# Optimization experiments

Measured on AMD Instinct MI355X. Metric: run time of the kernel, lower is better.

## Reference

```python
import jax, jax.numpy as jnp
import numpy as np

B, D, N, H = 16, 512, 4096, 4
HD = D // H  # head_dim = 128


def conv1(x, w, b):
    # 1x1 Conv1d == per-position matmul. x: (b, Cin, L), w: (Cout, Cin), b: (Cout,)
    return jnp.einsum('oi,bin->bon', w, x) + b[:, None]


def ln_c(x, g, b, eps=1e-5):
    # TransLN: LayerNorm over the channel axis (axis=1) at every position.
    m = jnp.mean(x, axis=1, keepdims=True)
    v = jnp.var(x, axis=1, keepdims=True)
    return (x - m) * jax.lax.rsqrt(v + eps) * g[:, None] + b[:, None]


def gelu(x):
    return jax.nn.gelu(x, approximate=False)  # torch nn.GELU default = exact erf


def setup_inputs() -> dict:
    key = jax.random.key(0)
    ks = iter(jax.random.split(key, 40))

    def rn(*shape):
        return jax.random.normal(next(ks), shape, jnp.float32) * 0.02

    inp = {
        'group_token': jax.random.normal(next(ks), (B, D, 2), jnp.float32),
        'x': jax.random.normal(next(ks), (B, D, N), jnp.float32),
        # mlp_s: Mlp(2, D//2) -> Conv1d(2, D//2), GELU, Conv1d(D//2, 2)
        'ws1_w': rn(D // 2, 2), 'ws1_b': jnp.zeros(D // 2, jnp.float32),
        'ws2_w': rn(2, D // 2), 'ws2_b': jnp.zeros(2, jnp.float32),
        # mlp_c: Mlp(D, 4D)
        'wc1_w': rn(4 * D, D), 'wc1_b': jnp.zeros(4 * D, jnp.float32),
        'wc2_w': rn(D, 4 * D), 'wc2_b': jnp.zeros(D, jnp.float32),
        # proj q/k/v: Conv1d(D, D)
        'q_w': rn(D, D), 'q_b': jnp.zeros(D, jnp.float32),
        'k_w': rn(D, D), 'k_b': jnp.zeros(D, jnp.float32),
        'v_w': rn(D, D), 'v_b': jnp.zeros(D, jnp.float32),
        'merge_w': rn(D, D), 'merge_b': jnp.zeros(D, jnp.float32),
        # mlp = MLP([2D, 2D, D], do_bn=False): Conv1d(2D,2D), GELU, Conv1d(2D,D)
        'm1_w': rn(2 * D, 2 * D), 'm1_b': jnp.zeros(2 * D, jnp.float32),
        'm2_w': rn(D, 2 * D), 'm2_b': jnp.zeros(D, jnp.float32),
        # norm0 / norm1 LayerNorm(D)
        'n0_g': jnp.ones(D, jnp.float32), 'n0_b': jnp.zeros(D, jnp.float32),
        'n1_g': jnp.ones(D, jnp.float32), 'n1_b': jnp.zeros(D, jnp.float32),
        # grouping: D->64->16->4->2 with TransLN+GELU between, softmax(axis=1)
        'g1_w': rn(64, D), 'g1_b': jnp.zeros(64, jnp.float32),
        'gl1_g': jnp.ones(64, jnp.float32), 'gl1_b': jnp.zeros(64, jnp.float32),
        'g2_w': rn(16, 64), 'g2_b': jnp.zeros(16, jnp.float32),
        'gl2_g': jnp.ones(16, jnp.float32), 'gl2_b': jnp.zeros(16, jnp.float32),
        'g3_w': rn(4, 16), 'g3_b': jnp.zeros(4, jnp.float32),
        'gl3_g': jnp.ones(4, jnp.float32), 'gl3_b': jnp.zeros(4, jnp.float32),
        'g4_w': rn(2, 4), 'g4_b': jnp.zeros(2, jnp.float32),
    }
    return inp


def reference(group_token, x, ws1_w, ws1_b, ws2_w, ws2_b, wc1_w, wc1_b, wc2_w, wc2_b,
              q_w, q_b, k_w, k_b, v_w, v_b, merge_w, merge_b,
              m1_w, m1_b, m2_w, m2_b, n0_g, n0_b, n1_g, n1_b,
              g1_w, g1_b, gl1_g, gl1_b, g2_w, g2_b, gl2_g, gl2_b,
              g3_w, g3_b, gl3_g, gl3_b, g4_w, g4_b):
    b = x.shape[0]
    # group_token: (b, D, 2)
    gt_t = jnp.swapaxes(group_token, 1, 2)                    # (b, 2, D)
    s = conv1(gelu(conv1(gt_t, ws1_w, ws1_b)), ws2_w, ws2_b)  # (b, 2, D)
    gt = group_token + jnp.swapaxes(s, 1, 2)
    gt = gt + conv1(gelu(conv1(gt, wc1_w, wc1_b)), wc2_w, wc2_b)

    # projections; torch view(b, head_dim, heads, -1) splits channels as (HD, H)
    q = conv1(x, q_w, q_b).reshape(b, HD, H, N)
    k = conv1(gt, k_w, k_b).reshape(b, HD, H, 2)
    v = conv1(gt, v_w, v_b).reshape(b, HD, H, 2)

    attn = jax.nn.softmax(jnp.einsum('bdhn,bdhm->bhnm', q, k) * (HD ** -0.5), axis=-1)
    out = jnp.einsum('bhnm,bdhm->bdhn', attn, v).reshape(b, D, N)
    out = conv1(out, merge_w, merge_b)

    h = jnp.concatenate([x, ln_c(out, n0_g, n0_b)], axis=1)   # (b, 2D, N)
    h = conv1(gelu(conv1(h, m1_w, m1_b)), m2_w, m2_b)         # (b, D, N)
    xd = x + ln_c(h, n1_g, n1_b)

    g = gelu(ln_c(conv1(xd, g1_w, g1_b), gl1_g, gl1_b))
    g = gelu(ln_c(conv1(g, g2_w, g2_b), gl2_g, gl2_b))
    g = gelu(ln_c(conv1(g, g3_w, g3_b), gl3_g, gl3_b))
    g = jax.nn.softmax(conv1(g, g4_w, g4_b), axis=1)          # (b, 2, N)
    return g[:, 0, :]                                         # (b, N)
```

## Files before the change

### kernel.cpp

```cpp
#include <hip/hip_runtime.h>
#include <math.h>

typedef unsigned short u16;
typedef unsigned int u32;
typedef __attribute__((ext_vector_type(8))) short bfrag;
typedef __attribute__((ext_vector_type(4))) float f32x4;

__device__ __forceinline__ float gelu_f(float x){
  return 0.5f * x * (1.0f + erff(x * 0.70710678118654752440f));
}
__device__ __forceinline__ u16 f2bf(float f){
  union { float f; unsigned int i; } c; c.f = f;
  unsigned int i = c.i;
  return (u16)((i + 0x7FFFu + ((i >> 16) & 1u)) >> 16);
}
__device__ __forceinline__ float bf2f(u16 u){
  union { unsigned int i; float f; } c; c.i = ((unsigned int)u) << 16; return c.f;
}

__device__ __forceinline__ void gload_lds16(const u16* g, u16* l){
  __builtin_amdgcn_global_load_lds(
      (const __attribute__((address_space(1))) u32*)(g),
      (__attribute__((address_space(3))) u32*)(l),
      16, 0, 0);
}

struct F8 { float v[8]; };
__device__ __forceinline__ F8 load8f(const float* p){
  float4 a = *(const float4*)p; float4 b = *(const float4*)(p + 4);
  F8 r; r.v[0]=a.x; r.v[1]=a.y; r.v[2]=a.z; r.v[3]=a.w;
  r.v[4]=b.x; r.v[5]=b.y; r.v[6]=b.z; r.v[7]=b.w; return r;
}

#define PRE_STRIDE 4624

__global__ __launch_bounds__(256) void k0a_mlps(
    const float* __restrict__ gtok,
    const float* __restrict__ ws1_w, const float* __restrict__ ws1_b,
    const float* __restrict__ ws2_w, const float* __restrict__ ws2_b,
    float* __restrict__ GT1)
{
  __shared__ float sw1[256][2]; __shared__ float sb1[256];
  __shared__ float sw2[2][256];
  const int b = blockIdx.x;
  const int t = threadIdx.x;
  sw1[t][0] = ws1_w[2*t]; sw1[t][1] = ws1_w[2*t+1];
  sb1[t] = ws1_b[t];
  sw2[0][t] = ws2_w[t]; sw2[1][t] = ws2_w[256+t];
  __syncthreads();
  const int j = blockIdx.y*256 + t;
  const float a0 = gtok[b*1024 + 2*j], a1 = gtok[b*1024 + 2*j + 1];
  float s0 = ws2_b[0], s1 = ws2_b[1];
  #pragma unroll 4
  for (int o = 0; o < 256; ++o){
    float h = gelu_f(sw1[o][0]*a0 + sw1[o][1]*a1 + sb1[o]);
    s0 += sw2[0][o]*h; s1 += sw2[1][o]*h;
  }
  GT1[b*1024 + 2*j]     = a0 + s0;
  GT1[b*1024 + 2*j + 1] = a1 + s1;
}

__global__ __launch_bounds__(256) void k0b_fc1(
    const float* __restrict__ GT1,
    const float* __restrict__ wc1_w, const float* __restrict__ wc1_b,
    float* __restrict__ HID)
{
  __shared__ float g[1024];
  const int b = blockIdx.x;
  const int t = threadIdx.x;
  for (int i = t; i < 1024; i += 256) g[i] = GT1[b*1024 + i];
  __syncthreads();
  const int o = blockIdx.y*256 + t;
  const float* wr = wc1_w + (size_t)o*512;
  float acc0 = wc1_b[o], acc1 = acc0;
  for (int d = 0; d < 512; d += 8){
    F8 w = load8f(wr + d);
    #pragma unroll
    for (int i = 0; i < 8; ++i){
      acc0 += w.v[i]*g[(d+i)*2];
      acc1 += w.v[i]*g[(d+i)*2+1];
    }
  }
  HID[b*4096 + o]        = gelu_f(acc0);
  HID[b*4096 + 2048 + o] = gelu_f(acc1);
}

__global__ __launch_bounds__(256) void k0c_fc2(
    const float* __restrict__ GT1, const float* __restrict__ HID,
    const float* __restrict__ wc2_w, const float* __restrict__ wc2_b,
    float* __restrict__ GT2)
{
  __shared__ float h0[2048], h1[2048];
  const int b = blockIdx.x;
  const int t = threadIdx.x;
  for (int i = t; i < 2048; i += 256){
    h0[i] = HID[b*4096 + i]; h1[i] = HID[b*4096 + 2048 + i];
  }
  __syncthreads();
  const int d = blockIdx.y*256 + t;
  const float* wr = wc2_w + (size_t)d*2048;
  float acc0 = wc2_b[d], acc1 = acc0;
  for (int o = 0; o < 2048; o += 8){
    F8 w = load8f(wr + o);
    #pragma unroll
    for (int i = 0; i < 8; ++i){
      acc0 += w.v[i]*h0[o+i];
      acc1 += w.v[i]*h1[o+i];
    }
  }
  GT2[b*1024 + 2*d]     = GT1[b*1024 + 2*d]     + acc0;
  GT2[b*1024 + 2*d + 1] = GT1[b*1024 + 2*d + 1] + acc1;
}

__global__ __launch_bounds__(256) void k0d_kv(
    const float* __restrict__ GT2,
    const float* __restrict__ k_w,
    const float* __restrict__ v_w, const float* __restrict__ v_b,
    float* __restrict__ DK, float* __restrict__ DV, float* __restrict__ V1L)
{
  __shared__ float g[1024];
  const int b = blockIdx.x;
  const int t = threadIdx.x;
  for (int i = t; i < 1024; i += 256) g[i] = GT2[b*1024 + i];
  __syncthreads();
  const int c = blockIdx.y*256 + t;
  const float* kr = k_w + (size_t)c*512;
  const float* vr = v_w + (size_t)c*512;
  float k0a=0.f,k1a=0.f,v0a=0.f,v1a=0.f;
  for (int d = 0; d < 512; d += 8){
    F8 kw = load8f(kr + d); F8 vw = load8f(vr + d);
    #pragma unroll
    for (int i = 0; i < 8; ++i){
      float g0 = g[(d+i)*2], g1 = g[(d+i)*2+1];
      k0a += kw.v[i]*g0; k1a += kw.v[i]*g1;
      v0a += vw.v[i]*g0; v1a += vw.v[i]*g1;
    }
  }
  DK[b*512 + c]  = k0a - k1a;
  DV[b*512 + c]  = v0a - v1a;
  V1L[b*512 + c] = v1a + v_b[c];
}

__global__ __launch_bounds__(256) void k0e_qpre(
    const float* __restrict__ DK,
    const float* __restrict__ q_w, const float* __restrict__ q_b,
    float* __restrict__ PRE)
{
  __shared__ float dkl[512];
  const int b = blockIdx.x;
  const int t = threadIdx.x;
  for (int i = t; i < 512; i += 256) dkl[i] = DK[b*512 + i];
  __syncthreads();
  const int i = blockIdx.y*256 + t;
  float w0=0.f,w1=0.f,w2=0.f,w3=0.f;
  for (int c = 0; c < 512; c += 4){
    w0 += dkl[c]  *q_w[(size_t)(c)  *512 + i];
    w1 += dkl[c+1]*q_w[(size_t)(c+1)*512 + i];
    w2 += dkl[c+2]*q_w[(size_t)(c+2)*512 + i];
    w3 += dkl[c+3]*q_w[(size_t)(c+3)*512 + i];
  }
  float* P = PRE + (size_t)b * PRE_STRIDE;
  P[0*512+i]=w0; P[1*512+i]=w1; P[2*512+i]=w2; P[3*512+i]=w3;
  if (blockIdx.y == 0 && t < 4){
    float bsum = 0.f;
    for (int c = t; c < 512; c += 4) bsum += dkl[c]*q_b[c];
    P[2048 + t] = bsum;
  }
}

__global__ __launch_bounds__(256) void k0f_mpre(
    const float* __restrict__ DV, const float* __restrict__ V1L,
    const float* __restrict__ merge_w, const float* __restrict__ merge_b,
    float* __restrict__ PRE)
{
  __shared__ float dvl[512], v1ll[512];
  const int b = blockIdx.x;
  const int t = threadIdx.x;
  for (int i = t; i < 512; i += 256){
    dvl[i] = DV[b*512 + i]; v1ll[i] = V1L[b*512 + i];
  }
  __syncthreads();
  const int r = blockIdx.y*256 + t;
  const float* mw = merge_w + (size_t)r*512;
  float ab = merge_b[r];
  float mh[4] = {0.f,0.f,0.f,0.f};
  for (int c = 0; c < 512; c += 8){
    F8 w = load8f(mw + c);
    #pragma unroll
    for (int i = 0; i < 8; ++i){
      ab += w.v[i]*v1ll[c+i];
      mh[i&3] += w.v[i]*dvl[c+i];
    }
  }
  float* P = PRE + (size_t)b * PRE_STRIDE;
  P[2064 + r] = ab;
  *(float4*)&P[2576 + r*4] = make_float4(mh[0],mh[1],mh[2],mh[3]);
}

__global__ __launch_bounds__(256) void kcvt(const float* __restrict__ s,
                                            u16* __restrict__ d, int n8)
{
  int g = blockIdx.x*256 + threadIdx.x;
  if (g >= n8) return;
  F8 v = load8f(s + (size_t)g*8);
  u16 o[8];
  #pragma unroll
  for (int i=0;i<8;++i) o[i] = f2bf(v.v[i]);
  *(uint4*)(d + (size_t)g*8) = *(uint4*)o;
}

__global__ __launch_bounds__(256) void kcvt_dup(const float* __restrict__ g1w,
                                                u16* __restrict__ out)
{
  int idx = blockIdx.x*256 + threadIdx.x;
  int r = idx >> 10, k = idx & 1023;
  out[idx] = f2bf(g1w[r*512 + (k & 511)]);
}

__global__ __launch_bounds__(256) void k1_fused(
    const float* __restrict__ x, const float* __restrict__ PRE,
    const float* __restrict__ n0_g, const float* __restrict__ n0_b,
    int j0_global, u16* __restrict__ XYbT)
{
  __shared__ float wd[4][512];
  __shared__ float bs[512];
  __shared__ float Mm[512][4];
  __shared__ float gam[512], bet[512];
  __shared__ float beta4[4];
  __shared__ float part[4][2][128];
  __shared__ float pstat[2][2][128];
  const int tid = threadIdx.x;
  const int cid = tid & 127;
  const int half = tid >> 7;
  const int jl = blockIdx.x*128 + cid;
  const int jg = j0_global + jl;
  const int b = jg >> 12, n = jg & 4095;
  const float* P = PRE + (size_t)b * PRE_STRIDE;
  for (int i = tid; i < 2048; i += 256) wd[i>>9][i&511] = P[i];
  if (tid < 4) beta4[tid] = P[2048 + tid];
  for (int i = tid; i < 512; i += 256){
    bs[i] = P[2064 + i]; gam[i] = n0_g[i]; bet[i] = n0_b[i];
  }
  for (int i = tid; i < 2048; i += 256) Mm[i>>2][i&3] = P[2576 + i];
  __syncthreads();
  const float* xc = x + (size_t)b*2097152 + n;
  u16* col = XYbT + (size_t)jl*1024;
  const int ibase = half*256;
  float l0=0.f, l1=0.f, l2=0.f, l3=0.f;
  for (int i0 = 0; i0 < 256; i0 += 8){
    u16 ob[8];
    #pragma unroll
    for (int m = 0; m < 8; ++m){
      int i = ibase + i0 + m;
      float xv = xc[(size_t)i*4096];
      ob[m] = f2bf(xv);
      l0 += wd[0][i]*xv; l1 += wd[1][i]*xv;
      l2 += wd[2][i]*xv; l3 += wd[3][i]*xv;
    }
    *(uint4*)&col[ibase + i0] = *(uint4*)ob;
  }
  part[0][half][cid] = l0; part[1][half][cid] = l1;
  part[2][half][cid] = l2; part[3][half][cid] = l3;
  __syncthreads();
  l0 = part[0][0][cid] + part[0][1][cid] + beta4[0];
  l1 = part[1][0][cid] + part[1][1][cid] + beta4[1];
  l2 = part[2][0][cid] + part[2][1][cid] + beta4[2];
  l3 = part[3][0][cid] + part[3][1][cid] + beta4[3];
  const float sc = 0.0883883476483184405f;
  float p0 = 1.f/(1.f+expf(-sc*l0));
  float p1 = 1.f/(1.f+expf(-sc*l1));
  float p2 = 1.f/(1.f+expf(-sc*l2));
  float p3 = 1.f/(1.f+expf(-sc*l3));
  float s=0.f, s2=0.f;
  for (int c = ibase; c < ibase + 256; ++c){
    float m = bs[c] + Mm[c][0]*p0 + Mm[c][1]*p1 + Mm[c][2]*p2 + Mm[c][3]*p3;
    s += m; s2 += m*m;
  }
  pstat[0][half][cid] = s; pstat[1][half][cid] = s2;
  __syncthreads();
  s  = pstat[0][0][cid] + pstat[0][1][cid];
  s2 = pstat[1][0][cid] + pstat[1][1][cid];
  float mean = s*(1.f/512.f);
  float rs = rsqrtf(s2*(1.f/512.f) - mean*mean + 1e-5f);
  for (int c0 = ibase; c0 < ibase + 256; c0 += 8){
    u16 ob[8];
    #pragma unroll
    for (int m = 0; m < 8; ++m){
      int c = c0 + m;
      float v = bs[c] + Mm[c][0]*p0 + Mm[c][1]*p1 + Mm[c][2]*p2 + Mm[c][3]*p3;
      ob[m] = f2bf((v - mean)*rs*gam[c] + bet[c]);
    }
    *(uint4*)&col[512 + c0] = *(uint4*)ob;
  }
}

__global__ __launch_bounds__(256) void mfma_gemm_p(
    const u16* __restrict__ Wb, const float* __restrict__ bias,
    const u16* __restrict__ XT, int K, int M,
    u16* __restrict__ Out, int do_gelu, int log2nbi)
{
  __shared__ __align__(16) u16 SH[2][8192];
  const int tid = threadIdx.x;
  const int lane = tid & 63;
  const int wv = __builtin_amdgcn_readfirstlane(tid >> 6);
  const int id = blockIdx.x;
  const int bi = (id >> 3) & ((1 << log2nbi) - 1);
  const int bj = (id & 7) + 8 * (id >> (3 + log2nbi));
  const int roff = (wv >> 1) * 64;
  const int noff = (wv & 1) * 64;
  const int lm = lane & 15, quad = lane >> 4;

  f32x4 acc[4][4];
  #pragma unroll
  for (int i=0;i<4;++i){
    #pragma unroll
    for (int j=0;j<4;++j) acc[i][j] = (f32x4){0.f,0.f,0.f,0.f};
  }

  const int r16 = lane >> 2;
  const int kc  = (lane & 3) * 8;
  const u16* aG = Wb + (size_t)(bi*128 + wv*32 + r16)*K + kc;
  const u16* bG = XT + (size_t)(bj*128 + wv*32 + r16)*1024 + kc;
  const int aOff = wv*1024;
  const int bOff = 4096 + wv*1024;

#define GP_STAGE(base, kk) do { \
    gload_lds16(aG + (kk),                 (base) + aOff); \
    gload_lds16(aG + (size_t)16*K + (kk),  (base) + aOff + 512); \
    gload_lds16(bG + (kk),                 (base) + bOff); \
    gload_lds16(bG + 16*1024 + (kk),       (base) + bOff + 512); \
  } while(0)

#define GP_COMPUTE(base) do { \
    bfrag av[4], bv[4]; \
    _Pragma("unroll") \
    for (int i=0;i<4;++i) \
      av[i] = *(const bfrag*)&(base)[(roff + 16*i + lm)*32 + quad*8]; \
    _Pragma("unroll") \
    for (int j=0;j<4;++j) \
      bv[j] = *(const bfrag*)&(base)[4096 + (noff + 16*j + lm)*32 + quad*8]; \
    _Pragma("unroll") \
    for (int i=0;i<4;++i){ \
      _Pragma("unroll") \
      for (int j=0;j<4;++j) \
        acc[i][j] = __builtin_amdgcn_mfma_f32_16x16x32_bf16(av[i], bv[j], acc[i][j], 0,0,0); \
    } \
  } while(0)

  u16* cur = &SH[0][0];
  u16* nxt = &SH[1][0];
  GP_STAGE(cur, 0);
  for (int k0 = 0; k0 + 32 < K; k0 += 32){
    GP_STAGE(nxt, k0 + 32);
    asm volatile("s_waitcnt vmcnt(4)" ::: "memory");
    __builtin_amdgcn_s_barrier();
    __builtin_amdgcn_sched_barrier(0);
    GP_COMPUTE(cur);
    __builtin_amdgcn_sched_barrier(0);
    __builtin_amdgcn_s_barrier();
    u16* t = cur; cur = nxt; nxt = t;
  }
  asm volatile("s_waitcnt vmcnt(0)" ::: "memory");
  __builtin_amdgcn_s_barrier();
  __builtin_amdgcn_sched_barrier(0);
  GP_COMPUTE(cur);
  __syncthreads();
#undef GP_STAGE
#undef GP_COMPUTE

  u16* Tt = &SH[0][0];
  #pragma unroll
  for (int p = 0; p < 2; ++p){
    if ((wv & 1) == p){
      #pragma unroll
      for (int i=0;i<4;++i){
        float4 bb = *(const float4*)&bias[bi*128 + roff + 16*i + quad*4];
        float b4[4] = {bb.x,bb.y,bb.z,bb.w};
        #pragma unroll
        for (int j=0;j<4;++j){
          int colr = 16*j + lm;
          #pragma unroll
          for (int s2=0;s2<2;++s2){
            float v0 = acc[i][j][2*s2]   + b4[2*s2];
            float v1 = acc[i][j][2*s2+1] + b4[2*s2+1];
            if (do_gelu){ v0 = gelu_f(v0); v1 = gelu_f(v1); }
            unsigned int dw = (unsigned int)f2bf(v0) | ((unsigned int)f2bf(v1) << 16);
            *(unsigned int*)&Tt[colr*136 + roff + 16*i + quad*4 + 2*s2] = dw;
          }
        }
      }
    }
    __syncthreads();
    {
      int c = tid >> 2, q = tid & 3;
      u16* dst = Out + (size_t)(bj*128 + p*64 + c)*M + bi*128 + q*32;
      const u16* src = &Tt[c*136 + q*32];
      #pragma unroll
      for (int m=0;m<2;++m){
        *(uint4*)(dst + m*8)      = *(const uint4*)(src + m*8);
        *(uint4*)(dst + 16 + m*8) = *(const uint4*)(src + 16 + m*8);
      }
    }
    __syncthreads();
  }
}

__global__ __launch_bounds__(256) void mfma_g64(
    const u16* __restrict__ Wg, const float* __restrict__ bias,
    const u16* __restrict__ XT, u16* __restrict__ Out)
{
  __shared__ __align__(16) u16 SH[2][10240];
  const int tid = threadIdx.x;
  const int lane = tid & 63;
  const int wv = __builtin_amdgcn_readfirstlane(tid >> 6);
  const int bj = blockIdx.x;
  const int lm = lane & 15, quad = lane >> 4;

  f32x4 acc[4][4];
  #pragma unroll
  for (int i=0;i<4;++i){
    #pragma unroll
    for (int j=0;j<4;++j) acc[i][j] = (f32x4){0.f,0.f,0.f,0.f};
  }
  const int r16 = lane >> 2;
  const int kc  = (lane & 3) * 8;
  const u16* aG = Wg + (size_t)(wv*16 + r16)*1024 + kc;
  const u16* bG = XT + (size_t)(bj*256 + wv*64 + r16)*1024 + kc;
  const int aOff = wv*512;
  const int bOff = 2048 + wv*2048;

#define G64_STAGE(base, kk) do { \
    gload_lds16(aG + (kk), (base) + aOff); \
    _Pragma("unroll") \
    for (int g = 0; g < 4; ++g) \
      gload_lds16(bG + (size_t)(g*16)*1024 + (kk), (base) + bOff + g*512); \
  } while(0)

#define G64_COMPUTE(base) do { \
    bfrag av[4], bv[4]; \
    _Pragma("unroll") \
    for (int i=0;i<4;++i) \
      av[i] = *(const bfrag*)&(base)[(16*i + lm)*32 + quad*8]; \
    _Pragma("unroll") \
    for (int j=0;j<4;++j) \
      bv[j] = *(const bfrag*)&(base)[2048 + (wv*64 + 16*j + lm)*32 + quad*8]; \
    _Pragma("unroll") \
    for (int i=0;i<4;++i){ \
      _Pragma("unroll") \
      for (int j=0;j<4;++j) \
        acc[i][j] = __builtin_amdgcn_mfma_f32_16x16x32_bf16(av[i], bv[j], acc[i][j], 0,0,0); \
    } \
  } while(0)

  u16* cur = &SH[0][0];
  u16* nxt = &SH[1][0];
  G64_STAGE(cur, 0);
  for (int k0 = 0; k0 + 32 < 1024; k0 += 32){
    G64_STAGE(nxt, k0 + 32);
    asm volatile("s_waitcnt vmcnt(5)" ::: "memory");
    __builtin_amdgcn_s_barrier();
    __builtin_amdgcn_sched_barrier(0);
    G64_COMPUTE(cur);
    __builtin_amdgcn_sched_barrier(0);
    __builtin_amdgcn_s_barrier();
    u16* t = cur; cur = nxt; nxt = t;
  }
  asm volatile("s_waitcnt vmcnt(0)" ::: "memory");
  __builtin_amdgcn_s_barrier();
  __builtin_amdgcn_sched_barrier(0);
  G64_COMPUTE(cur);
  __syncthreads();
#undef G64_STAGE
#undef G64_COMPUTE

  u16* Tg = &SH[0][0];
  #pragma unroll
  for (int i=0;i<4;++i){
    float4 bb = *(const float4*)&bias[16*i + quad*4];
    float b4[4] = {bb.x,bb.y,bb.z,bb.w};
    #pragma unroll
    for (int j=0;j<4;++j){
      int col = wv*64 + 16*j + lm;
      #pragma unroll
      for (int s2=0;s2<2;++s2){
        float v0 = acc[i][j][2*s2]   + b4[2*s2];
        float v1 = acc[i][j][2*s2+1] + b4[2*s2+1];
        unsigned int dw = (unsigned int)f2bf(v0) | ((unsigned int)f2bf(v1) << 16);
        *(unsigned int*)&Tg[col*72 + 16*i + quad*4 + 2*s2] = dw;
      }
    }
  }
  __syncthreads();
  {
    u16* dst = Out + (size_t)(bj*256 + tid)*64;
    const u16* src = &Tg[tid*72];
    #pragma unroll
    for (int m=0;m<8;++m)
      *(uint4*)(dst + m*8) = *(const uint4*)(src + m*8);
  }
}

__global__ __launch_bounds__(256) void k_lnT(
    const u16* __restrict__ t2T,
    const float* __restrict__ gamma, const float* __restrict__ beta,
    u16* __restrict__ XYbT)
{
  __shared__ float gam[512], bet[512];
  const int tid = threadIdx.x;
  for (int c = tid; c < 512; c += 256){ gam[c]=gamma[c]; bet[c]=beta[c]; }
  __syncthreads();
  const int lane = tid & 63, wv = tid >> 6;
  const int j = blockIdx.x*4 + wv;
  uint4 w = *(const uint4*)(t2T + (size_t)j*512 + lane*8);
  const u16* wp = (const u16*)&w;
  float vv[8];
  #pragma unroll
  for (int m=0;m<8;++m) vv[m] = bf2f(wp[m]);
  float s = 0.f, s2 = 0.f;
  #pragma unroll
  for (int m=0;m<8;++m){ s += vv[m]; s2 += vv[m]*vv[m]; }
  #pragma unroll
  for (int off = 32; off; off >>= 1){
    s  += __shfl_xor(s,  off, 64);
    s2 += __shfl_xor(s2, off, 64);
  }
  float mean = s*(1.f/512.f);
  float rs = rsqrtf(s2*(1.f/512.f) - mean*mean + 1e-5f);
  u16 ob[8];
  #pragma unroll
  for (int m=0;m<8;++m){
    int c = lane*8 + m;
    ob[m] = f2bf((vv[m]-mean)*rs*gam[c] + bet[c]);
  }
  *(uint4*)&XYbT[(size_t)j*1024 + 512 + lane*8] = *(uint4*)ob;
}

__global__ __launch_bounds__(256) void k_head(
    const u16* __restrict__ G,
    const float* __restrict__ gl1_g, const float* __restrict__ gl1_b,
    const float* __restrict__ g2_w, const float* __restrict__ g2_b,
    const float* __restrict__ gl2_g, const float* __restrict__ gl2_b,
    const float* __restrict__ g3_w, const float* __restrict__ g3_b,
    const float* __restrict__ gl3_g, const float* __restrict__ gl3_b,
    const float* __restrict__ g4_w, const float* __restrict__ g4_b, int has_g4b,
    float* __restrict__ Outp, int j0_global)
{
  __shared__ float L1g[64], L1b[64];
  __shared__ float W2[16][64], B2v[16], G2v[16], T2v[16];
  __shared__ float W3[4][16], B3v[4], G3v[4], T3v[4];
  __shared__ float W4d[4]; __shared__ float b4d;
  const int tid = threadIdx.x;
  if (tid < 64){ L1g[tid]=gl1_g[tid]; L1b[tid]=gl1_b[tid]; }
  for (int i = tid; i < 1024; i += 256) W2[i>>6][i&63] = g2_w[i];
  if (tid < 16){ B2v[tid]=g2_b[tid]; G2v[tid]=gl2_g[tid]; T2v[tid]=gl2_b[tid]; }
  if (tid < 64) W3[tid>>4][tid&15] = g3_w[tid];
  if (tid < 4){ B3v[tid]=g3_b[tid]; G3v[tid]=gl3_g[tid]; T3v[tid]=gl3_b[tid];
                W4d[tid] = g4_w[tid] - g4_w[4+tid]; }
  if (tid == 0) b4d = has_g4b ? (g4_b[0] - g4_b[1]) : 0.f;
  __syncthreads();
  const int jl = blockIdx.x*256 + tid;
  const u16* gc = G + (size_t)jl*64;
  float a1[64]; float s=0.f;
  #pragma unroll
  for (int c0=0;c0<64;c0+=8){
    uint4 w = *(const uint4*)(gc + c0);
    const u16* wp = (const u16*)&w;
    #pragma unroll
    for (int m=0;m<8;++m){ a1[c0+m] = bf2f(wp[m]); s += a1[c0+m]; }
  }
  float m = s*(1.f/64.f); float s2=0.f;
  #pragma unroll
  for (int c=0;c<64;++c){ float d=a1[c]-m; s2+=d*d; }
  float rs = rsqrtf(s2*(1.f/64.f)+1e-5f);
  #pragma unroll
  for (int c=0;c<64;++c) a1[c] = gelu_f((a1[c]-m)*rs*L1g[c]+L1b[c]);

  float a2[16]; s=0.f;
  #pragma unroll
  for (int i=0;i<16;++i){
    float acc = B2v[i];
    #pragma unroll
    for (int o=0;o<64;++o) acc += W2[i][o]*a1[o];
    a2[i]=acc; s+=acc;
  }
  m = s*(1.f/16.f); s2=0.f;
  #pragma unroll
  for (int i=0;i<16;++i){ float d=a2[i]-m; s2+=d*d; }
  rs = rsqrtf(s2*(1.f/16.f)+1e-5f);
  float a2g[16];
  #pragma unroll
  for (int i=0;i<16;++i) a2g[i] = gelu_f((a2[i]-m)*rs*G2v[i]+T2v[i]);

  float a3[4]; s=0.f;
  #pragma unroll
  for (int i=0;i<4;++i){
    float acc=B3v[i];
    #pragma unroll
    for (int o=0;o<16;++o) acc += W3[i][o]*a2g[o];
    a3[i]=acc; s+=acc;
  }
  m = s*0.25f; s2=0.f;
  #pragma unroll
  for (int i=0;i<4;++i){ float d=a3[i]-m; s2+=d*d; }
  rs = rsqrtf(s2*0.25f+1e-5f);
  float z = b4d;
  #pragma unroll
  for (int i=0;i<4;++i) z += W4d[i]*gelu_f((a3[i]-m)*rs*G3v[i]+T3v[i]);
  Outp[j0_global + jl] = 1.f/(1.f+expf(-z));
}

extern "C" void kernel_launch(void* const* d_in, const int* in_sizes, int n_in,
                              void* d_out, int out_size, void* d_ws, size_t ws_size,
                              hipStream_t stream)
{
  const float* gtok  = (const float*)d_in[0];
  const float* x     = (const float*)d_in[1];
  const float* ws1_w = (const float*)d_in[2];
  const float* ws1_b = (const float*)d_in[3];
  const float* ws2_w = (const float*)d_in[4];
  const float* ws2_b = (const float*)d_in[5];
  const float* wc1_w = (const float*)d_in[6];
  const float* wc1_b = (const float*)d_in[7];
  const float* wc2_w = (const float*)d_in[8];
  const float* wc2_b = (const float*)d_in[9];
  const float* q_w   = (const float*)d_in[10];
  const float* q_b   = (const float*)d_in[11];
  const float* k_w   = (const float*)d_in[12];
  const float* v_w   = (const float*)d_in[14];
  const float* v_b   = (const float*)d_in[15];
  const float* merge_w = (const float*)d_in[16];
  const float* merge_b = (const float*)d_in[17];
  const float* m1_w  = (const float*)d_in[18];
  const float* m1_b  = (const float*)d_in[19];
  const float* m2_w  = (const float*)d_in[20];
  const float* m2_b  = (const float*)d_in[21];
  const float* n0_g  = (const float*)d_in[22];
  const float* n0_b  = (const float*)d_in[23];
  const float* n1_g  = (const float*)d_in[24];
  const float* n1_b  = (const float*)d_in[25];
  const float* g1_w  = (const float*)d_in[26];
  const float* g1_b  = (const float*)d_in[27];
  const float* gl1_g = (const float*)d_in[28];
  const float* gl1_b = (const float*)d_in[29];
  const float* g2_w  = (const float*)d_in[30];
  const float* g2_b  = (const float*)d_in[31];
  const float* gl2_g = (const float*)d_in[32];
  const float* gl2_b = (const float*)d_in[33];
  const float* g3_w  = (const float*)d_in[34];
  const float* g3_b  = (const float*)d_in[35];
  const float* gl3_g = (const float*)d_in[36];
  const float* gl3_b = (const float*)d_in[37];
  const float* g4_w  = (const float*)d_in[38];
  const float* g4_b  = (n_in > 39) ? (const float*)d_in[39] : nullptr;

  const int TOT = 65536;
  const size_t PRE_BYTES = (size_t)16 * PRE_STRIDE * 4;
  const size_t GT1_B = 65536, HID_B = 262144, GT2_B = 65536;
  const size_t DK_B = 32768, DV_B = 32768, V1L_B = 32768;
  const size_t WB1_B = (size_t)1024*1024*2;
  const size_t WB2_B = (size_t)512*1024*2;
  const size_t WG_B  = (size_t)64*1024*2;
  const size_t FIXED = PRE_BYTES + GT1_B + HID_B + GT2_B + DK_B + DV_B + V1L_B
                     + WB1_B + WB2_B + WG_B;
  int C = 65536;
  while (C > 4096 && FIXED + (size_t)5248*C > ws_size) C >>= 1;
  const int nch = TOT / C;

  char* wsb = (char*)d_ws;
  size_t off = 0;
  float* PRE = (float*)(wsb + off); off += PRE_BYTES;
  float* GT1 = (float*)(wsb + off); off += GT1_B;
  float* HID = (float*)(wsb + off); off += HID_B;
  float* GT2 = (float*)(wsb + off); off += GT2_B;
  float* DK  = (float*)(wsb + off); off += DK_B;
  float* DV  = (float*)(wsb + off); off += DV_B;
  float* V1L = (float*)(wsb + off); off += V1L_B;
  u16* Wb1   = (u16*)(wsb + off);   off += WB1_B;
  u16* Wb2   = (u16*)(wsb + off);   off += WB2_B;
  u16* Wg    = (u16*)(wsb + off);   off += WG_B;
  u16* XYbT  = (u16*)(wsb + off);   off += (size_t)2048*C;
  u16* T1bT  = (u16*)(wsb + off);   off += (size_t)2048*C;
  u16* T2bT  = (u16*)(wsb + off);   off += (size_t)1024*C;
  u16* bufG  = (u16*)(wsb + off);   off += (size_t)128*C;

  dim3 blk(256);
  hipLaunchKernelGGL(kcvt, dim3(512), blk, 0, stream, m1_w, Wb1, 1024*1024/8);
  hipLaunchKernelGGL(kcvt, dim3(256), blk, 0, stream, m2_w, Wb2, 512*1024/8);
  hipLaunchKernelGGL(kcvt_dup, dim3(256), blk, 0, stream, g1_w, Wg);
  hipLaunchKernelGGL(k0a_mlps, dim3(16,2), blk, 0, stream,
      gtok, ws1_w, ws1_b, ws2_w, ws2_b, GT1);
  hipLaunchKernelGGL(k0b_fc1, dim3(16,8), blk, 0, stream, GT1, wc1_w, wc1_b, HID);
  hipLaunchKernelGGL(k0c_fc2, dim3(16,2), blk, 0, stream, GT1, HID, wc2_w, wc2_b, GT2);
  hipLaunchKernelGGL(k0d_kv,  dim3(16,2), blk, 0, stream, GT2, k_w, v_w, v_b, DK, DV, V1L);
  hipLaunchKernelGGL(k0e_qpre, dim3(16,2), blk, 0, stream, DK, q_w, q_b, PRE);
  hipLaunchKernelGGL(k0f_mpre, dim3(16,2), blk, 0, stream, DV, V1L, merge_w, merge_b, PRE);

  for (int ch = 0; ch < nch; ++ch){
    const int j0 = ch * C;
    hipLaunchKernelGGL(k1_fused, dim3(C/128), blk, 0, stream,
        x, PRE, n0_g, n0_b, j0, XYbT);
    hipLaunchKernelGGL(mfma_gemm_p, dim3(8*(C/128)), blk, 0, stream,
        Wb1, m1_b, XYbT, 1024, 1024, T1bT, 1, 3);
    hipLaunchKernelGGL(mfma_gemm_p, dim3(4*(C/128)), blk, 0, stream,
        Wb2, m2_b, T1bT, 1024, 512, T2bT, 0, 2);
    hipLaunchKernelGGL(k_lnT, dim3(C/4), blk, 0, stream, T2bT, n1_g, n1_b, XYbT);
    hipLaunchKernelGGL(mfma_g64, dim3(C/256), blk, 0, stream, Wg, g1_b, XYbT, bufG);
    hipLaunchKernelGGL(k_head, dim3(C/256), blk, 0, stream,
        bufG, gl1_g, gl1_b, g2_w, g2_b, gl2_g, gl2_b,
        g3_w, g3_b, gl3_g, gl3_b,
        g4_w, g4_b ? g4_b : g4_w, g4_b ? 1 : 0, (float*)d_out, j0);
  }
}
```

Baseline: 1.103 ms.

## Triple-buffer GEMM K loops, halve g64 tile width, replace erf with polynomial

Both MFMA GEMM kernels move from double to triple buffering of LDS stages, so two K-steps of global loads stay in flight and waitcnt thresholds are adjusted to match. The g64 kernel narrows its column tile from 256 to 128 positions per block, doubling the grid to raise occupancy and parallelism. GELU's erff is replaced by an Abramowitz-Stegun polynomial with fast rcp and exp, which cuts transcendental cost but adds about 1e-7 absolute erf error. The larger LDS footprint in mfma_gemm_p may reduce how many blocks fit per CU.

```diff
diff --git a/kernel.cpp b/kernel.cpp
--- a/kernel.cpp
+++ b/kernel.cpp
@@ -7,7 +7,13 @@
 typedef __attribute__((ext_vector_type(4))) float f32x4;
 
 __device__ __forceinline__ float gelu_f(float x){
-  return 0.5f * x * (1.0f + erff(x * 0.70710678118654752440f));
+  float z = fabsf(x) * 0.70710678118654752440f;
+  float t = __builtin_amdgcn_rcpf(1.0f + 0.3275911f*z);
+  float p = t*(0.254829592f + t*(-0.284496736f + t*(1.421413741f
+            + t*(-1.453152027f + t*1.061405429f))));
+  float e = __expf(-z*z);
+  float er = copysignf(1.0f - p*e, x);
+  return 0.5f * x * (1.0f + er);
 }
 __device__ __forceinline__ u16 f2bf(float f){
   union { float f; unsigned int i; } c; c.f = f;
@@ -299,7 +305,7 @@
     const u16* __restrict__ XT, int K, int M,
     u16* __restrict__ Out, int do_gelu, int log2nbi)
 {
-  __shared__ __align__(16) u16 SH[2][8192];
+  __shared__ __align__(16) u16 SH[3][8192];
   const int tid = threadIdx.x;
   const int lane = tid & 63;
   const int wv = __builtin_amdgcn_readfirstlane(tid >> 6);
@@ -347,23 +353,29 @@
     } \
   } while(0)
 
-  u16* cur = &SH[0][0];
-  u16* nxt = &SH[1][0];
-  GP_STAGE(cur, 0);
-  for (int k0 = 0; k0 + 32 < K; k0 += 32){
-    GP_STAGE(nxt, k0 + 32);
-    asm volatile("s_waitcnt vmcnt(4)" ::: "memory");
+  u16* b0 = &SH[0][0];
+  u16* b1 = &SH[1][0];
+  u16* b2 = &SH[2][0];
+  GP_STAGE(b0, 0);
+  GP_STAGE(b1, 32);
+  for (int k0 = 0; k0 + 64 < K; k0 += 32){
+    GP_STAGE(b2, k0 + 64);
+    asm volatile("s_waitcnt vmcnt(8)" ::: "memory");
     __builtin_amdgcn_s_barrier();
     __builtin_amdgcn_sched_barrier(0);
-    GP_COMPUTE(cur);
+    GP_COMPUTE(b0);
     __builtin_amdgcn_sched_barrier(0);
     __builtin_amdgcn_s_barrier();
-    u16* t = cur; cur = nxt; nxt = t;
-  }
+    u16* t = b0; b0 = b1; b1 = b2; b2 = t;
+  }
+  asm volatile("s_waitcnt vmcnt(4)" ::: "memory");
+  __builtin_amdgcn_s_barrier();
+  __builtin_amdgcn_sched_barrier(0);
+  GP_COMPUTE(b0);
   asm volatile("s_waitcnt vmcnt(0)" ::: "memory");
   __builtin_amdgcn_s_barrier();
   __builtin_amdgcn_sched_barrier(0);
-  GP_COMPUTE(cur);
+  GP_COMPUTE(b1);
   __syncthreads();
 #undef GP_STAGE
 #undef GP_COMPUTE
@@ -409,66 +421,71 @@
     const u16* __restrict__ Wg, const float* __restrict__ bias,
     const u16* __restrict__ XT, u16* __restrict__ Out)
 {
-  __shared__ __align__(16) u16 SH[2][10240];
+  __shared__ __align__(16) u16 SH[3][6144];
   const int tid = threadIdx.x;
   const int lane = tid & 63;
   const int wv = __builtin_amdgcn_readfirstlane(tid >> 6);
   const int bj = blockIdx.x;
   const int lm = lane & 15, quad = lane >> 4;
 
-  f32x4 acc[4][4];
+  f32x4 acc[4][2];
   #pragma unroll
   for (int i=0;i<4;++i){
     #pragma unroll
-    for (int j=0;j<4;++j) acc[i][j] = (f32x4){0.f,0.f,0.f,0.f};
+    for (int j=0;j<2;++j) acc[i][j] = (f32x4){0.f,0.f,0.f,0.f};
   }
   const int r16 = lane >> 2;
   const int kc  = (lane & 3) * 8;
   const u16* aG = Wg + (size_t)(wv*16 + r16)*1024 + kc;
-  const u16* bG = XT + (size_t)(bj*256 + wv*64 + r16)*1024 + kc;
+  const u16* bG = XT + (size_t)(bj*128 + wv*32 + r16)*1024 + kc;
   const int aOff = wv*512;
-  const int bOff = 2048 + wv*2048;
+  const int bOff = 2048 + wv*1024;
 
 #define G64_STAGE(base, kk) do { \
-    gload_lds16(aG + (kk), (base) + aOff); \
-    _Pragma("unroll") \
-    for (int g = 0; g < 4; ++g) \
-      gload_lds16(bG + (size_t)(g*16)*1024 + (kk), (base) + bOff + g*512); \
+    gload_lds16(aG + (kk),             (base) + aOff); \
+    gload_lds16(bG + (kk),             (base) + bOff); \
+    gload_lds16(bG + 16*1024 + (kk),   (base) + bOff + 512); \
   } while(0)
 
 #define G64_COMPUTE(base) do { \
-    bfrag av[4], bv[4]; \
+    bfrag av[4], bv[2]; \
     _Pragma("unroll") \
     for (int i=0;i<4;++i) \
       av[i] = *(const bfrag*)&(base)[(16*i + lm)*32 + quad*8]; \
     _Pragma("unroll") \
-    for (int j=0;j<4;++j) \
-      bv[j] = *(const bfrag*)&(base)[2048 + (wv*64 + 16*j + lm)*32 + quad*8]; \
+    for (int j=0;j<2;++j) \
+      bv[j] = *(const bfrag*)&(base)[2048 + (wv*32 + 16*j + lm)*32 + quad*8]; \
     _Pragma("unroll") \
     for (int i=0;i<4;++i){ \
       _Pragma("unroll") \
-      for (int j=0;j<4;++j) \
+      for (int j=0;j<2;++j) \
         acc[i][j] = __builtin_amdgcn_mfma_f32_16x16x32_bf16(av[i], bv[j], acc[i][j], 0,0,0); \
     } \
   } while(0)
 
-  u16* cur = &SH[0][0];
-  u16* nxt = &SH[1][0];
-  G64_STAGE(cur, 0);
-  for (int k0 = 0; k0 + 32 < 1024; k0 += 32){
-    G64_STAGE(nxt, k0 + 32);
-    asm volatile("s_waitcnt vmcnt(5)" ::: "memory");
+  u16* b0 = &SH[0][0];
+  u16* b1 = &SH[1][0];
+  u16* b2 = &SH[2][0];
+  G64_STAGE(b0, 0);
+  G64_STAGE(b1, 32);
+  for (int k0 = 0; k0 + 64 < 1024; k0 += 32){
+    G64_STAGE(b2, k0 + 64);
+    asm volatile("s_waitcnt vmcnt(6)" ::: "memory");
     __builtin_amdgcn_s_barrier();
     __builtin_amdgcn_sched_barrier(0);
-    G64_COMPUTE(cur);
+    G64_COMPUTE(b0);
     __builtin_amdgcn_sched_barrier(0);
     __builtin_amdgcn_s_barrier();
-    u16* t = cur; cur = nxt; nxt = t;
-  }
+    u16* t = b0; b0 = b1; b1 = b2; b2 = t;
+  }
+  asm volatile("s_waitcnt vmcnt(3)" ::: "memory");
+  __builtin_amdgcn_s_barrier();
+  __builtin_amdgcn_sched_barrier(0);
+  G64_COMPUTE(b0);
   asm volatile("s_waitcnt vmcnt(0)" ::: "memory");
   __builtin_amdgcn_s_barrier();
   __builtin_amdgcn_sched_barrier(0);
-  G64_COMPUTE(cur);
+  G64_COMPUTE(b1);
   __syncthreads();
 #undef G64_STAGE
 #undef G64_COMPUTE
@@ -479,8 +496,8 @@
     float4 bb = *(const float4*)&bias[16*i + quad*4];
     float b4[4] = {bb.x,bb.y,bb.z,bb.w};
     #pragma unroll
-    for (int j=0;j<4;++j){
-      int col = wv*64 + 16*j + lm;
+    for (int j=0;j<2;++j){
+      int col = wv*32 + 16*j + lm;
       #pragma unroll
       for (int s2=0;s2<2;++s2){
         float v0 = acc[i][j][2*s2]   + b4[2*s2];
@@ -492,10 +509,11 @@
   }
   __syncthreads();
   {
-    u16* dst = Out + (size_t)(bj*256 + tid)*64;
-    const u16* src = &Tg[tid*72];
-    #pragma unroll
-    for (int m=0;m<8;++m)
+    int c = tid >> 1, q = tid & 1;
+    u16* dst = Out + (size_t)(bj*128 + c)*64 + q*32;
+    const u16* src = &Tg[c*72 + q*32];
+    #pragma unroll
+    for (int m=0;m<4;++m)
       *(uint4*)(dst + m*8) = *(const uint4*)(src + m*8);
   }
 }
@@ -704,7 +722,7 @@
     hipLaunchKernelGGL(mfma_gemm_p, dim3(4*(C/128)), blk, 0, stream,
         Wb2, m2_b, T1bT, 1024, 512, T2bT, 0, 2);
     hipLaunchKernelGGL(k_lnT, dim3(C/4), blk, 0, stream, T2bT, n1_g, n1_b, XYbT);
-    hipLaunchKernelGGL(mfma_g64, dim3(C/256), blk, 0, stream, Wg, g1_b, XYbT, bufG);
+    hipLaunchKernelGGL(mfma_g64, dim3(C/128), blk, 0, stream, Wg, g1_b, XYbT, bufG);
     hipLaunchKernelGGL(k_head, dim3(C/256), blk, 0, stream,
         bufG, gl1_g, gl1_b, g2_w, g2_b, gl2_g, gl2_b,
         g3_w, g3_b, gl3_g, gl3_b,
```

Result: faster. 1.028 ms (-6.8%).
